# Performance work log

Measured on AMD Instinct MI355X. Metric: run time of the kernel, lower is better.

The kernel has to match this reference:

```python
import math
import jax, jax.numpy as jnp
import numpy as np

B, S, D, H, E = 4, 1024, 1024, 16, 8
HD = D // H


def gelu_new(x):
    # BERT/GPT tanh-approx GELU (NewGELUActivation)
    c = math.sqrt(2.0 / math.pi)
    return 0.5 * x * (1.0 + jnp.tanh(c * (x + 0.044715 * x ** 3)))


def setup_inputs() -> dict:
    key = jax.random.key(0)
    ks = jax.random.split(key, 12)
    s = 0.02
    return {
        "x": jax.random.normal(ks[0], (B, S, D), jnp.float32),
        "Wq": jax.random.normal(ks[1], (D, D), jnp.float32) * s,
        "bq": jnp.zeros((D,), jnp.float32),
        "Wk": jax.random.normal(ks[2], (D, D), jnp.float32) * s,
        "bk": jnp.zeros((D,), jnp.float32),
        "Wv": jax.random.normal(ks[3], (D, D), jnp.float32) * s,
        "bv": jnp.zeros((D,), jnp.float32),
        "Wg": jax.random.normal(ks[4], (D, E), jnp.float32) * s,
        "bg": jnp.zeros((E,), jnp.float32),
        "W1": jax.random.normal(ks[5], (E, D, D), jnp.float32) * s,
        "b1": jnp.zeros((E, D), jnp.float32),
        "W2": jax.random.normal(ks[6], (E, D, D), jnp.float32) * s,
        "b2": jnp.zeros((E, D), jnp.float32),
    }


def reference(x, Wq, bq, Wk, bk, Wv, bv, Wg, bg, W1, b1, W2, b2):
    b = x.shape[0]
    # ---- Attention (faithful to original: no head transpose, so attention
    # is computed ACROSS HEADS per token: scores are [B,S,H,H]) ----
    Q = (x @ Wq + bq).reshape(b, -1, H, HD)
    K = (x @ Wk + bk).reshape(b, -1, H, HD)
    V = (x @ Wv + bv).reshape(b, -1, H, HD)
    scores = jnp.einsum('bsqd,bskd->bsqk', Q, K) / (HD ** 0.5)  # [B,S,H,H]
    attn = jax.nn.softmax(scores, axis=-1)
    out = jnp.einsum('bsqk,bskd->bsqd', attn, V)  # [B,S,H,HD]
    # torch: out.transpose(1,2).contiguous().view(B,-1,H*HD)
    a = jnp.transpose(out, (0, 2, 1, 3)).reshape(b, -1, D)  # [B,S,D]

    # ---- ComplexMoE: dense all-experts + sequence-mean gating ----
    gates = jax.nn.softmax(a.mean(axis=1) @ Wg + bg, axis=-1)  # [B,E]
    h = gelu_new(jnp.einsum('bsd,edh->bseh', a, W1) + b1)       # [B,S,E,D]
    eo = jnp.einsum('bseh,ehf->bsef', h, W2) + b2               # [B,S,E,D]
    return jnp.einsum('be,bsed->bsd', gates, eo)                # [B,S,D]
```

## Files before the change

### kernel.cpp

```cpp
#include <hip/hip_runtime.h>
#include <stdint.h>

#define AS1 __attribute__((address_space(1)))
#define AS3 __attribute__((address_space(3)))

typedef short v8s __attribute__((ext_vector_type(8)));
typedef float v4f __attribute__((ext_vector_type(4)));

__device__ __forceinline__ float b2f(unsigned short u) {
  return __uint_as_float(((unsigned int)u) << 16);
}
__device__ __forceinline__ unsigned short f2bu(float f) {
  unsigned int u = __float_as_uint(f);
  u += 0x7fffu + ((u >> 16) & 1u);
  return (unsigned short)(u >> 16);
}

__device__ __forceinline__ void gload16(const void* g, const void* l) {
  __builtin_amdgcn_global_load_lds(
      (const AS1 void*)(uintptr_t)g,
      (AS3 void*)(unsigned)(uintptr_t)l,
      16, 0, 0);
}

#define BAR __builtin_amdgcn_s_barrier()
#define VMC4 asm volatile("s_waitcnt vmcnt(4)" ::: "memory")
#define VMC0 asm volatile("s_waitcnt vmcnt(0)" ::: "memory")

__global__ __launch_bounds__(256)
void transpose_cvt(const float* __restrict__ src, long long srcZ,
                   unsigned short* __restrict__ dst, long long dstZ, int ld_dst,
                   int K, int N)
{
  __shared__ float t[64][65];
  const int e = blockIdx.z;
  src += (long long)e * srcZ;
  dst += (long long)e * dstZ;
  const int k0 = blockIdx.y * 64, n0 = blockIdx.x * 64;
  const int tr  = threadIdx.x >> 4;
  const int tc4 = (threadIdx.x & 15) * 4;
#pragma unroll
  for (int p = 0; p < 4; ++p) {
    float4 v = *(const float4*)(src + (long long)(k0 + tr + p * 16) * N + n0 + tc4);
    t[tr + p * 16][tc4 + 0] = v.x;
    t[tr + p * 16][tc4 + 1] = v.y;
    t[tr + p * 16][tc4 + 2] = v.z;
    t[tr + p * 16][tc4 + 3] = v.w;
  }
  __syncthreads();
#pragma unroll
  for (int p = 0; p < 4; ++p) {
    const int n = tr + p * 16;
    ushort4 o;
    o.x = f2bu(t[tc4 + 0][n]);
    o.y = f2bu(t[tc4 + 1][n]);
    o.z = f2bu(t[tc4 + 2][n]);
    o.w = f2bu(t[tc4 + 3][n]);
    *(ushort4*)(dst + (long long)(n0 + n) * ld_dst + k0 + tc4) = o;
  }
}

__global__ __launch_bounds__(256)
void cvt_f32_bf16(const float* __restrict__ src, unsigned short* __restrict__ dst, int n)
{
  const int i = (blockIdx.x * 256 + threadIdx.x) * 4;
  if (i >= n) return;
  float4 v = *(const float4*)(src + i);
  ushort4 o;
  o.x = f2bu(v.x); o.y = f2bu(v.y); o.z = f2bu(v.z); o.w = f2bu(v.w);
  *(ushort4*)(dst + i) = o;
}

template<int MH>
__device__ __forceinline__ void read_a(v8s af[4][2],
    const unsigned short* pa, int wm, int rswz)
{
#pragma unroll
  for (int i = 0; i < 4; ++i)
#pragma unroll
    for (int s = 0; s < 2; ++s)
      af[i][s] = *(const v8s*)(pa + MH*8192 + ((((wm*4 + i)*2 + s) << 9) | rswz));
}

template<int NH>
__device__ __forceinline__ void read_b(v8s bfr[2][2],
    const unsigned short* pb, int wn, int rswz)
{
#pragma unroll
  for (int j = 0; j < 2; ++j)
#pragma unroll
    for (int s = 0; s < 2; ++s)
      bfr[j][s] = *(const v8s*)(pb + NH*8192 + ((((wn*2 + j)*2 + s) << 9) | rswz));
}

template<int MH, int NH>
__device__ __forceinline__ void quad_mfma(v4f acc[8][4], v8s af[4][2], v8s bfr[2][2])
{
  __builtin_amdgcn_s_setprio(1);
#pragma unroll
  for (int i = 0; i < 4; ++i)
#pragma unroll
    for (int j = 0; j < 2; ++j)
#pragma unroll
      for (int s = 0; s < 2; ++s)
        acc[MH*4+i][NH*2+j] = __builtin_amdgcn_mfma_f32_16x16x32_bf16(
            af[i][s], bfr[j][s], acc[MH*4+i][NH*2+j], 0, 0, 0);
  __builtin_amdgcn_s_setprio(0);
}

#define STAGE(G, LD, LDSBASE, GROW0, KT) do { \
    gload16((G) + (long long)((GROW0) + sRow) * (LD) + (KT) + sCol, \
            (LDSBASE) + w512); \
    gload16((G) + (long long)((GROW0) + 64 + sRow) * (LD) + (KT) + sCol, \
            (LDSBASE) + 4096 + w512); \
  } while (0)

template<int EPI>
__global__ __launch_bounds__(512, 2)
void gemm256(const unsigned short* __restrict__ A, int lda,
             const unsigned short* __restrict__ Bt, int ldb,
             const float* __restrict__ bias,
             void* __restrict__ out0, unsigned short* __restrict__ pbs,
             int kLen, const float* __restrict__ gates)
{
  __shared__ __align__(16) unsigned short lds[65536];
  unsigned short* As0 = lds;
  unsigned short* As1 = lds + 16384;
  unsigned short* Bs0 = lds + 32768;
  unsigned short* Bs1 = lds + 49152;

  const int tid  = threadIdx.x;
  const int lane = tid & 63;
  const int w    = tid >> 6;
  const int wm   = w >> 2;
  const int wn   = w & 3;
  const int m0   = blockIdx.y * 256;
  const int n0   = blockIdx.x * 256;
  const int z    = blockIdx.z;
  const int kBase = (EPI == 3) ? z * kLen : 0;

  const int sRow = (w >> 1) * 16 + (lane >> 2);
  const int sCol = (w & 1) * 32 + (((lane & 3) * 8) ^ (((lane >> 5) & 1) << 4));
  const int rr   = lane & 15;
  const int kgrp = lane >> 4;
  const int rswz = (rr * 32 + kgrp * 8) ^ ((rr & 8) << 1);
  const int w512 = w * 512;

  v4f acc[8][4] = {};
  v8s af[4][2], blo[2][2], bhi[2][2];

  const int iters = kLen >> 7;

  STAGE(A,  lda, As0,        m0,       kBase);
  STAGE(A,  lda, As0 + 8192, m0 + 128, kBase);
  STAGE(Bt, ldb, Bs0,        n0,       kBase);
  STAGE(Bt, ldb, Bs0 + 8192, n0 + 128, kBase);
  STAGE(A,  lda, As1,        m0,       kBase + 64);
  STAGE(Bt, ldb, Bs1,        n0,       kBase + 64);
  VMC4;
  BAR;

  for (int it = 0; it < iters; ++it) {
    const bool nl = (it != iters - 1);
    const int k0t = kBase + it * 128;
    const int kT1 = k0t + 64, kT2 = k0t + 128, kT3 = k0t + 192;

    read_a<0>(af, As0, wm, rswz);
    read_b<0>(blo, Bs0, wn, rswz);
    read_b<1>(bhi, Bs0, wn, rswz);
    STAGE(A,  lda, As1 + 8192, m0 + 128, kT1);
    STAGE(Bt, ldb, Bs1 + 8192, n0 + 128, kT1);
    BAR;
    quad_mfma<0,0>(acc, af, blo);
    quad_mfma<0,1>(acc, af, bhi);
    BAR;
    read_a<1>(af, As0, wm, rswz);
    if (nl) { STAGE(A, lda, As0, m0, kT2); STAGE(Bt, ldb, Bs0, n0, kT2); }
    BAR;
    quad_mfma<1,0>(acc, af, blo);
    quad_mfma<1,1>(acc, af, bhi);
    if (nl) { VMC4; } else { VMC0; }
    BAR;
    read_a<0>(af, As1, wm, rswz);
    read_b<0>(blo, Bs1, wn, rswz);
    read_b<1>(bhi, Bs1, wn, rswz);
    if (nl) { STAGE(A, lda, As0 + 8192, m0 + 128, kT2); STAGE(Bt, ldb, Bs0 + 8192, n0 + 128, kT2); }
    BAR;
    quad_mfma<0,0>(acc, af, blo);
    quad_mfma<0,1>(acc, af, bhi);
    BAR;
    read_a<1>(af, As1, wm, rswz);
    if (nl) { STAGE(A, lda, As1, m0, kT3); STAGE(Bt, ldb, Bs1, n0, kT3); }
    BAR;
    quad_mfma<1,0>(acc, af, blo);
    quad_mfma<1,1>(acc, af, bhi);
    if (nl) VMC4;
    BAR;
  }

  const int lr4 = (lane >> 4) * 4;
  const int lc  = lane & 15;
  float gate = 0.f;
  if (EPI == 1) gate = gates[(m0 >> 10) * 8 + (n0 >> 10)];

#pragma unroll
  for (int mi = 0; mi < 8; ++mi) {
    const int rowb = m0 + (mi >> 2) * 128 + wm * 64 + (mi & 3) * 16 + lr4;
#pragma unroll
    for (int nj = 0; nj < 4; ++nj) {
      const int col = n0 + (nj >> 1) * 128 + wn * 32 + (nj & 1) * 16 + lc;
#pragma unroll
      for (int r = 0; r < 4; ++r) {
        const int row = rowb + r;
        float v = acc[mi][nj][r];
        if (EPI == 0) {
          v += bias[col];
          const int which = col >> 10;
          ((unsigned short*)out0)[(long long)which * 4194304 + (long long)row * 1024 + (col & 1023)] = f2bu(v);
        } else if (EPI == 1) {
          v += bias[col];
          float u = 0.7978845608028654f * (v + 0.044715f * v * v * v);
          u = fminf(fmaxf(u, -15.f), 15.f);
          float e2 = __expf(2.f * u);
          float th = (e2 - 1.f) / (e2 + 1.f);
          ((unsigned short*)out0)[(long long)row * 8192 + col] = f2bu(gate * 0.5f * v * (1.f + th));
        } else {
          if (z == 0) ((float*)out0)[(long long)row * 1024 + col] = v;
          else pbs[(long long)(z - 1) * 4194304 + (long long)row * 1024 + col] = f2bu(v);
        }
      }
    }
  }
}

__global__ __launch_bounds__(256)
void reduce3(float* __restrict__ out, const unsigned short* __restrict__ pb,
             const float* __restrict__ bias2)
{
  const int i = (blockIdx.x * 256 + threadIdx.x) * 4;
  const int b = i >> 20;
  const int n = i & 1023;
  float4 a = *(const float4*)(out + i);
  ushort4 p0 = *(const ushort4*)(pb + i);
  ushort4 p1 = *(const ushort4*)(pb + 4194304 + i);
  ushort4 p2 = *(const ushort4*)(pb + 8388608 + i);
  float4 bb = *(const float4*)(bias2 + b * 1024 + n);
  a.x += b2f(p0.x) + b2f(p1.x) + b2f(p2.x) + bb.x;
  a.y += b2f(p0.y) + b2f(p1.y) + b2f(p2.y) + bb.y;
  a.z += b2f(p0.z) + b2f(p1.z) + b2f(p2.z) + bb.z;
  a.w += b2f(p0.w) + b2f(p1.w) + b2f(p2.w) + bb.w;
  *(float4*)(out + i) = a;
}

__global__ __launch_bounds__(256)
void attn_kernel(const unsigned short* __restrict__ Qb,
                 const unsigned short* __restrict__ Kb,
                 const unsigned short* __restrict__ Vb,
                 unsigned short* __restrict__ a)
{
  const int token = blockIdx.x;
  const int b = token >> 10, s = token & 1023;
  __shared__ float Qs[16][65], Ks[16][65], Vs[16][65];
  __shared__ float attn_s[16][17];
  const int t = threadIdx.x;
  const long long base = (long long)token * 1024;

  {
    const int i0 = t * 4;
    const int hh = i0 >> 6, dd = i0 & 63;
    ushort4 qv = *(const ushort4*)(Qb + base + i0);
    ushort4 kv = *(const ushort4*)(Kb + base + i0);
    ushort4 vv = *(const ushort4*)(Vb + base + i0);
    Qs[hh][dd+0]=b2f(qv.x); Qs[hh][dd+1]=b2f(qv.y); Qs[hh][dd+2]=b2f(qv.z); Qs[hh][dd+3]=b2f(qv.w);
    Ks[hh][dd+0]=b2f(kv.x); Ks[hh][dd+1]=b2f(kv.y); Ks[hh][dd+2]=b2f(kv.z); Ks[hh][dd+3]=b2f(kv.w);
    Vs[hh][dd+0]=b2f(vv.x); Vs[hh][dd+1]=b2f(vv.y); Vs[hh][dd+2]=b2f(vv.z); Vs[hh][dd+3]=b2f(vv.w);
  }
  __syncthreads();

  const int q = t >> 4, k = t & 15;
  float sc = 0.f;
#pragma unroll
  for (int d = 0; d < 64; ++d) sc += Qs[q][d] * Ks[k][d];
  sc *= 0.125f;
  float mx = sc;
#pragma unroll
  for (int m = 1; m < 16; m <<= 1) mx = fmaxf(mx, __shfl_xor(mx, m, 64));
  float ex = __expf(sc - mx);
  float sum = ex;
#pragma unroll
  for (int m = 1; m < 16; m <<= 1) sum += __shfl_xor(sum, m, 64);
  attn_s[q][k] = ex / sum;
  __syncthreads();

  const int hd = t & 63;
  const int wv = t >> 6;
#pragma unroll
  for (int r = 0; r < 4; ++r) {
    const int qq = wv * 4 + r;
    float o = 0.f;
#pragma unroll
    for (int kk = 0; kk < 16; ++kk) o += attn_s[qq][kk] * Vs[kk][hd];
    a[(long long)b * 1048576 + (long long)(qq * 64 + (s >> 4)) * 1024 + (s & 15) * 64 + hd] = f2bu(o);
  }
}

__global__ __launch_bounds__(256)
void col_sum_part(const unsigned short* __restrict__ a, float* __restrict__ part)
{
  const int bx = blockIdx.x;
  const int b = bx >> 2;
  const int d = (bx & 3) * 256 + threadIdx.x;
  const int y = blockIdx.y;
  const unsigned short* p = a + (long long)b * 1048576 + (long long)y * 131072 + d;
  float s = 0.f;
  for (int i = 0; i < 128; ++i) s += b2f(p[i * 1024]);
  part[(y * 4 + b) * 1024 + d] = s;
}

__global__ __launch_bounds__(256)
void gates_bias2(const float* __restrict__ part,
                 const float* __restrict__ Wg,
                 const float* __restrict__ bg,
                 const float* __restrict__ b2,
                 float* __restrict__ gates,
                 float* __restrict__ bias2)
{
  __shared__ float am[4][1024];
  __shared__ float sg[4][8];
  const int t = threadIdx.x;

  for (int i = t; i < 4096; i += 256) {
    const int b = i >> 10, d = i & 1023;
    float s = 0.f;
#pragma unroll
    for (int y = 0; y < 8; ++y) s += part[(y * 4 + b) * 1024 + d];
    am[b][d] = s * (1.f / 1024.f);
  }
  __syncthreads();

  const int pair = t >> 3, subl = t & 7;
  const int b = pair >> 3, e = pair & 7;
  float s = 0.f;
  for (int d = subl * 128; d < subl * 128 + 128; ++d) s += am[b][d] * Wg[d * 8 + e];
#pragma unroll
  for (int m = 1; m < 8; m <<= 1) s += __shfl_xor(s, m, 64);
  if (subl == 0) sg[b][e] = s + bg[e];
  __syncthreads();

  if (t < 4) {
    float mx = -1e30f;
    for (int ee = 0; ee < 8; ++ee) mx = fmaxf(mx, sg[t][ee]);
    float g[8]; float ssum = 0.f;
    for (int ee = 0; ee < 8; ++ee) { g[ee] = __expf(sg[t][ee] - mx); ssum += g[ee]; }
    for (int ee = 0; ee < 8; ++ee) { sg[t][ee] = g[ee] / ssum; gates[t * 8 + ee] = sg[t][ee]; }
  }
  __syncthreads();

  for (int i = t; i < 4096; i += 256) {
    const int bb = i >> 10, n = i & 1023;
    float ss = 0.f;
#pragma unroll
    for (int ee = 0; ee < 8; ++ee) ss += sg[bb][ee] * b2[ee * 1024 + n];
    bias2[i] = ss;
  }
}

extern "C" void kernel_launch(void* const* d_in, const int* in_sizes, int n_in,
                              void* d_out, int out_size, void* d_ws, size_t ws_size,
                              hipStream_t stream) {
  const float* x  = (const float*)d_in[0];
  const float* Wq = (const float*)d_in[1];
  const float* bq = (const float*)d_in[2];
  const float* Wk = (const float*)d_in[3];
  const float* bk = (const float*)d_in[4];
  const float* Wv = (const float*)d_in[5];
  const float* bv = (const float*)d_in[6];
  const float* Wg = (const float*)d_in[7];
  const float* bg = (const float*)d_in[8];
  const float* W1 = (const float*)d_in[9];
  const float* b1 = (const float*)d_in[10];
  const float* W2 = (const float*)d_in[11];
  const float* b2 = (const float*)d_in[12];
  float* out = (float*)d_out;

  if (ws_size < (size_t)109300000) return;

  char* ws = (char*)d_ws;
  unsigned short* xb   = (unsigned short*)(ws + 0);
  unsigned short* Wqt  = (unsigned short*)(ws + 8388608);
  unsigned short* Qb   = (unsigned short*)(ws + 14680064);
  unsigned short* hs   = (unsigned short*)(ws + 0);
  unsigned short* abuf = (unsigned short*)(ws + 67108864);
  unsigned short* pbs  = (unsigned short*)(ws + 67108864);
  unsigned short* W1t  = (unsigned short*)(ws + 75497472);
  unsigned short* W2t  = (unsigned short*)(ws + 92274688);
  float* part  = (float*)(ws + 109051904);
  float* gates = (float*)(ws + 109051904 + 131072);
  float* bias2 = (float*)(ws + 109051904 + 131072 + 512);
  float* bqkv  = (float*)(ws + 109051904 + 131072 + 512 + 16384);

  dim3 tb(256);

  transpose_cvt<<<dim3(16,16,1), tb, 0, stream>>>(Wq, 0LL, Wqt,           0LL, 1024, 1024, 1024);
  transpose_cvt<<<dim3(16,16,1), tb, 0, stream>>>(Wk, 0LL, Wqt + 1048576, 0LL, 1024, 1024, 1024);
  transpose_cvt<<<dim3(16,16,1), tb, 0, stream>>>(Wv, 0LL, Wqt + 2097152, 0LL, 1024, 1024, 1024);
  transpose_cvt<<<dim3(16,16,8), tb, 0, stream>>>(W1, 1048576LL, W1t, 1048576LL, 1024, 1024, 1024);
  transpose_cvt<<<dim3(16,16,8), tb, 0, stream>>>(W2, 1048576LL, W2t, 1024LL,    8192, 1024, 1024);
  cvt_f32_bf16<<<4096, tb, 0, stream>>>(x, xb, 4194304);
  hipMemcpyAsync(bqkv,        bq, 4096, hipMemcpyDeviceToDevice, stream);
  hipMemcpyAsync(bqkv + 1024, bk, 4096, hipMemcpyDeviceToDevice, stream);
  hipMemcpyAsync(bqkv + 2048, bv, 4096, hipMemcpyDeviceToDevice, stream);

  gemm256<0><<<dim3(12,16,1), 512, 0, stream>>>(xb, 1024, Wqt, 1024, bqkv,
                                                Qb, nullptr, 1024, nullptr);
  attn_kernel<<<4096, tb, 0, stream>>>(Qb, Qb + 4194304, Qb + 8388608, abuf);
  col_sum_part<<<dim3(16,8), tb, 0, stream>>>(abuf, part);
  gates_bias2<<<1, tb, 0, stream>>>(part, Wg, bg, b2, gates, bias2);
  gemm256<1><<<dim3(32,16,1), 512, 0, stream>>>(abuf, 1024, W1t, 1024, b1,
                                                hs, nullptr, 1024, gates);
  gemm256<3><<<dim3(4,16,4), 512, 0, stream>>>(hs, 8192, W2t, 8192, nullptr,
                                               out, pbs, 2048, nullptr);
  reduce3<<<4096, tb, 0, stream>>>(out, pbs, bias2);
}
```

Measured before the change: 270.1 us.

## Interleave GEMM main loop into eight MFMA phases with finer-grained staged loads

Restructures the GEMM main loop from four phases of 32 MFMAs into eight phases of 16 MFMAs, each bracketed by barriers. One half-tile global-to-LDS stage is issued per phase, B fragment reads are split across phases, and the wait threshold drops from vmcnt(4) to vmcnt(2). The intent is to spread memory traffic more evenly across the compute and hide load latency better. In exchange it doubles the number of barriers per iteration, and the reordered stage timing must still respect the LDS buffer hazards.

```diff
diff --git a/kernel.cpp b/kernel.cpp
--- a/kernel.cpp
+++ b/kernel.cpp
@@ -24,7 +24,7 @@
 }
 
 #define BAR __builtin_amdgcn_s_barrier()
-#define VMC4 asm volatile("s_waitcnt vmcnt(4)" ::: "memory")
+#define VMC2 asm volatile("s_waitcnt vmcnt(2)" ::: "memory")
 #define VMC0 asm volatile("s_waitcnt vmcnt(0)" ::: "memory")
 
 __global__ __launch_bounds__(256)
@@ -94,7 +94,7 @@
 }
 
 template<int MH, int NH>
-__device__ __forceinline__ void quad_mfma(v4f acc[8][4], v8s af[4][2], v8s bfr[2][2])
+__device__ __forceinline__ void mfma16(v4f acc[8][4], v8s af[4][2], v8s bfr[2][2])
 {
   __builtin_amdgcn_s_setprio(1);
 #pragma unroll
@@ -147,7 +147,7 @@
   const int w512 = w * 512;
 
   v4f acc[8][4] = {};
-  v8s af[4][2], blo[2][2], bhi[2][2];
+  v8s af[4][2], b0[2][2], b1[2][2];
 
   const int iters = kLen >> 7;
 
@@ -156,8 +156,7 @@
   STAGE(Bt, ldb, Bs0,        n0,       kBase);
   STAGE(Bt, ldb, Bs0 + 8192, n0 + 128, kBase);
   STAGE(A,  lda, As1,        m0,       kBase + 64);
-  STAGE(Bt, ldb, Bs1,        n0,       kBase + 64);
-  VMC4;
+  VMC2;
   BAR;
 
   for (int it = 0; it < iters; ++it) {
@@ -166,35 +165,32 @@
     const int kT1 = k0t + 64, kT2 = k0t + 128, kT3 = k0t + 192;
 
     read_a<0>(af, As0, wm, rswz);
-    read_b<0>(blo, Bs0, wn, rswz);
-    read_b<1>(bhi, Bs0, wn, rswz);
-    STAGE(A,  lda, As1 + 8192, m0 + 128, kT1);
+    read_b<0>(b0, Bs0, wn, rswz);
+    STAGE(Bt, ldb, Bs1, n0, kT1);
+    BAR; mfma16<0,0>(acc, af, b0); BAR;
+    read_b<1>(b1, Bs0, wn, rswz);
     STAGE(Bt, ldb, Bs1 + 8192, n0 + 128, kT1);
-    BAR;
-    quad_mfma<0,0>(acc, af, blo);
-    quad_mfma<0,1>(acc, af, bhi);
-    BAR;
+    BAR; mfma16<0,1>(acc, af, b1); BAR;
     read_a<1>(af, As0, wm, rswz);
-    if (nl) { STAGE(A, lda, As0, m0, kT2); STAGE(Bt, ldb, Bs0, n0, kT2); }
-    BAR;
-    quad_mfma<1,0>(acc, af, blo);
-    quad_mfma<1,1>(acc, af, bhi);
-    if (nl) { VMC4; } else { VMC0; }
+    STAGE(A, lda, As1 + 8192, m0 + 128, kT1);
+    BAR; mfma16<1,1>(acc, af, b1); BAR;
+    if (nl) STAGE(A, lda, As0, m0, kT2);
+    BAR; mfma16<1,0>(acc, af, b0);
+    if (nl) { VMC2; } else { VMC0; }
     BAR;
     read_a<0>(af, As1, wm, rswz);
-    read_b<0>(blo, Bs1, wn, rswz);
-    read_b<1>(bhi, Bs1, wn, rswz);
-    if (nl) { STAGE(A, lda, As0 + 8192, m0 + 128, kT2); STAGE(Bt, ldb, Bs0 + 8192, n0 + 128, kT2); }
-    BAR;
-    quad_mfma<0,0>(acc, af, blo);
-    quad_mfma<0,1>(acc, af, bhi);
-    BAR;
+    read_b<0>(b0, Bs1, wn, rswz);
+    if (nl) STAGE(Bt, ldb, Bs0, n0, kT2);
+    BAR; mfma16<0,0>(acc, af, b0); BAR;
+    read_b<1>(b1, Bs1, wn, rswz);
+    if (nl) STAGE(Bt, ldb, Bs0 + 8192, n0 + 128, kT2);
+    BAR; mfma16<0,1>(acc, af, b1); BAR;
     read_a<1>(af, As1, wm, rswz);
-    if (nl) { STAGE(A, lda, As1, m0, kT3); STAGE(Bt, ldb, Bs1, n0, kT3); }
-    BAR;
-    quad_mfma<1,0>(acc, af, blo);
-    quad_mfma<1,1>(acc, af, bhi);
-    if (nl) VMC4;
+    if (nl) STAGE(A, lda, As0 + 8192, m0 + 128, kT2);
+    BAR; mfma16<1,1>(acc, af, b1); BAR;
+    if (nl) STAGE(A, lda, As1, m0, kT3);
+    BAR; mfma16<1,0>(acc, af, b0);
+    if (nl) { VMC2; }
     BAR;
   }
 
```

Result: no change. 266.9 us (-1.2%).
